# Optimization experiments

Hardware: AMD Instinct MI355X
Metric: run time of the kernel (lower is better)

## Reference

```python
import jax, jax.numpy as jnp
import numpy as np

K = 20
EPS = 1e-5


def _knn(x, k):
    # x: [B, C, N] -> indices of k nearest points, [B, N, k]
    sq = jnp.sum(x * x, axis=1)  # [B, N]
    neg_d2 = 2.0 * jnp.einsum('bcn,bcm->bnm', x, x) - sq[:, None, :] - sq[:, :, None]
    return jax.lax.top_k(neg_d2, k)[1]


def _graph_feature(x, idx):
    # x: [B, C, N], idx: [B, N, k] -> edge features [B, 2C, N, k]
    xT = x.transpose(0, 2, 1)  # [B, N, C]
    nbr = jax.vmap(lambda t, i: t[i])(xT, idx)  # [B, N, k, C]
    ctr = jnp.broadcast_to(xT[:, :, None, :], nbr.shape)
    f = jnp.concatenate([nbr - ctr, ctr], axis=-1)  # [B, N, k, 2C]
    return f.transpose(0, 3, 1, 2)


def _lrelu(x):
    return jnp.where(x > 0, x, 0.2 * x)


def _bn(x, g, b):
    # eval-mode BatchNorm with freshly-initialized running stats (mean=0, var=1)
    shp = (1, -1) + (1,) * (x.ndim - 2)
    return x * (g / jnp.sqrt(1.0 + EPS)).reshape(shp) + b.reshape(shp)


def _c2(x, w):  # 1x1 Conv2d, no bias
    return jnp.einsum('oi,bink->bonk', w, x)


def _c1(x, w):  # 1x1 Conv1d, no bias
    return jnp.einsum('oi,bin->bon', w, x)


def reference(coords, feats, w1, w2, w3, w4, w5, w6, w7, w8, w9,
              g15, b15, g6, b6, g7, b7, g8, b8):
    x0 = jnp.concatenate([coords.transpose(0, 2, 1), feats], axis=1)  # [B, 6, N]
    n = x0.shape[2]
    # EdgeConv block 1 (kNN on xyz only)
    x = _graph_feature(x0, _knn(x0[:, :3], K))  # [B, 12, N, k]
    x = _lrelu(_bn(_c2(x, w1), g15[0], b15[0]))
    x = _lrelu(_bn(_c2(x, w2), g15[1], b15[1]))
    x1 = jnp.max(x, axis=-1)  # [B, 64, N]
    # EdgeConv block 2 (dynamic kNN in feature space)
    x = _graph_feature(x1, _knn(x1, K))
    x = _lrelu(_bn(_c2(x, w3), g15[2], b15[2]))
    x = _lrelu(_bn(_c2(x, w4), g15[3], b15[3]))
    x2 = jnp.max(x, axis=-1)
    # EdgeConv block 3
    x = _graph_feature(x2, _knn(x2, K))
    x3 = jnp.max(_lrelu(_bn(_c2(x, w5), g15[4], b15[4])), axis=-1)
    # global embedding + per-point head
    xc = jnp.concatenate([x1, x2, x3], axis=1)  # [B, 192, N]
    x = _lrelu(_bn(_c1(xc, w6), g6, b6))  # [B, 1024, N]
    gmax = jnp.max(x, axis=-1, keepdims=True)
    x = jnp.concatenate([jnp.broadcast_to(gmax, (x.shape[0], x.shape[1], n)), x1, x2, x3], axis=1)  # [B,1216,N]
    x = _lrelu(_bn(_c1(x, w7), g7, b7))
    x = _lrelu(_bn(_c1(x, w8), g8, b8))
    # dropout is identity in eval mode
    x = _c1(x, w9)  # [B, 20, N]
    return x.transpose(0, 2, 1).reshape(-1, w9.shape[0])


def setup_inputs() -> dict:
    key = jax.random.key(0)
    ks = jax.random.split(key, 16)
    B, N, C = 8, 4096, 3
    s = 0.1
    return {
        'coords': jax.random.uniform(ks[0], (B, N, 3), jnp.float32),
        'feats': jax.random.normal(ks[1], (B, C, N), jnp.float32),
        'w1': s * jax.random.normal(ks[2], (64, 12), jnp.float32),
        'w2': s * jax.random.normal(ks[3], (64, 64), jnp.float32),
        'w3': s * jax.random.normal(ks[4], (64, 128), jnp.float32),
        'w4': s * jax.random.normal(ks[5], (64, 64), jnp.float32),
        'w5': s * jax.random.normal(ks[6], (64, 128), jnp.float32),
        'w6': s * jax.random.normal(ks[7], (1024, 192), jnp.float32),
        'w7': s * jax.random.normal(ks[8], (512, 1216), jnp.float32),
        'w8': s * jax.random.normal(ks[9], (256, 512), jnp.float32),
        'w9': s * jax.random.normal(ks[10], (20, 256), jnp.float32),
        'g15': jnp.ones((5, 64), jnp.float32),
        'b15': jnp.zeros((5, 64), jnp.float32),
        'g6': jnp.ones((1024,), jnp.float32),
        'b6': jnp.zeros((1024,), jnp.float32),
        'g7': jnp.ones((512,), jnp.float32),
        'b7': jnp.zeros((512,), jnp.float32),
        'g8': jnp.ones((256,), jnp.float32),
        'b8': jnp.zeros((256,), jnp.float32),
    }
```

## Files before the change

### kernel.cpp

```cpp
#include <hip/hip_runtime.h>
#include <math.h>

#define BB 8
#define NN 4096
#define KNN 20
#define EPSBN 1e-5f

__device__ __forceinline__ float lrelu(float x){ return x > 0.f ? x : 0.2f*x; }
__device__ __forceinline__ unsigned encf(float f){
  unsigned u = __float_as_uint(f);
  return (u & 0x80000000u) ? ~u : (u | 0x80000000u);
}
__device__ __forceinline__ float decf(unsigned u){
  return (u & 0x80000000u) ? __uint_as_float(u & 0x7fffffffu) : __uint_as_float(~u);
}
__device__ __forceinline__ float rdlane(float v, int l){
  return __uint_as_float(__builtin_amdgcn_readlane(__float_as_uint(v), l));
}

__global__ void prep_w(float* __restrict__ dst, const float* __restrict__ src,
                       int O, int I, int ld, int coff, const float* __restrict__ g){
  int tot = O*I;
  for(int t = blockIdx.x*blockDim.x + threadIdx.x; t < tot; t += gridDim.x*blockDim.x){
    int o = t % O, i = t / O;
    float s = g ? g[o] * (1.0f/sqrtf(1.0f+EPSBN)) : 1.0f;
    dst[(size_t)i*O + o] = src[(size_t)o*ld + coff + i] * s;
  }
}

__global__ void init_gmax(unsigned* __restrict__ g){
  int t = blockIdx.x*blockDim.x + threadIdx.x;
  if(t < BB*1024) g[t] = 0u;
}

__global__ void build_x0(const float* __restrict__ coords, const float* __restrict__ feats,
                         float* __restrict__ x0p){
  int p = blockIdx.x*blockDim.x + threadIdx.x;
  if(p >= BB*NN) return;
  int b = p / NN, n = p % NN;
  x0p[(size_t)p*6+0] = coords[(size_t)p*3+0];
  x0p[(size_t)p*6+1] = coords[(size_t)p*3+1];
  x0p[(size_t)p*6+2] = coords[(size_t)p*3+2];
  #pragma unroll
  for(int cc=0; cc<3; ++cc) x0p[(size_t)p*6+3+cc] = feats[((size_t)b*3+cc)*NN + n];
}

template<int D, int LD>
__global__ __launch_bounds__(512,4) void knn_kernel(const float* __restrict__ X, int coloff,
                                                    int* __restrict__ idxOut){
  constexpr int IG = 8;
  __shared__ float stage[2][IG][512];
  __shared__ float xi_s[IG][(D+3)&~3];
  __shared__ float sqi_s[IG];
  const int t = threadIdx.x;
  const int w = t >> 6, l = t & 63;
  const int b = blockIdx.x / (NN/IG);
  const int i0 = (blockIdx.x % (NN/IG)) * IG;
  const float* Xb = X + (size_t)b*NN*LD + coloff;

  for(int u = t; u < IG*D; u += 512) xi_s[u/D][u%D] = Xb[(size_t)(i0 + u/D)*LD + (u%D)];
  __syncthreads();
  if(t < IG){
    float s = 0.f;
    for(int d=0; d<D; ++d){ float v = xi_s[t][d]; s = fmaf(v, v, s); }
    sqi_s[t] = s;
  }
  __syncthreads();

  float v1=-INFINITY, v2=-INFINITY, v3=-INFINITY;
  int   j1=0x7fffffff, j2=0x7fffffff, j3=0x7fffffff;
  auto ins = [&](float v, int jj){
    bool b1 = v > v1, b2 = v > v2, b3 = v > v3;
    v3 = b3 ? (b2 ? v2 : v) : v3;
    j3 = b3 ? (b2 ? j2 : jj) : j3;
    v2 = b2 ? (b1 ? v1 : v) : v2;
    j2 = b2 ? (b1 ? j1 : jj) : j2;
    v1 = b1 ? v : v1;
    j1 = b1 ? jj : j1;
  };

  for(int s = 0; s < NN/512; ++s){
    const int j = s*512 + t;
    const float* row = Xb + (size_t)j*LD;
    float dot[IG];
    #pragma unroll
    for(int q=0;q<IG;++q) dot[q] = 0.f;
    float sqj = 0.f;
    if constexpr (D % 4 == 0){
      #pragma unroll
      for(int d0=0; d0<D; d0+=4){
        const float4 v = *reinterpret_cast<const float4*>(row + d0);
        sqj = fmaf(v.x,v.x,sqj); sqj = fmaf(v.y,v.y,sqj);
        sqj = fmaf(v.z,v.z,sqj); sqj = fmaf(v.w,v.w,sqj);
        #pragma unroll
        for(int q=0;q<IG;++q){
          const float4 xw = *reinterpret_cast<const float4*>(&xi_s[q][d0]);
          float a = dot[q];
          a = fmaf(v.x,xw.x,a); a = fmaf(v.y,xw.y,a);
          a = fmaf(v.z,xw.z,a); a = fmaf(v.w,xw.w,a);
          dot[q] = a;
        }
      }
    } else {
      #pragma unroll
      for(int d0=0; d0<D; ++d0){
        float v = row[d0];
        sqj = fmaf(v,v,sqj);
        #pragma unroll
        for(int q=0;q<IG;++q) dot[q] = fmaf(v, xi_s[q][d0], dot[q]);
      }
    }
    const int buf = s & 1;
    #pragma unroll
    for(int q=0;q<IG;++q)
      stage[buf][q][t] = 2.f*dot[q] - sqj - sqi_s[q];
    __syncthreads();
    {
      const float4 va = *reinterpret_cast<const float4*>(&stage[buf][w][4*l]);
      const int ja = s*512 + 4*l;
      ins(va.x, ja+0); ins(va.y, ja+1); ins(va.z, ja+2); ins(va.w, ja+3);
      const float4 vb = *reinterpret_cast<const float4*>(&stage[buf][w][256 + 4*l]);
      const int jb2 = s*512 + 256 + 4*l;
      ins(vb.x, jb2+0); ins(vb.y, jb2+1); ins(vb.z, jb2+2); ins(vb.w, jb2+3);
    }
  }

  int* outRow = idxOut + (size_t)(b*NN + i0 + w)*KNN;
  const float sqi = sqi_s[w];
  #pragma unroll 1
  for(int r=0;r<KNN;++r){
    float bv = v1; int bj = j1;
    #pragma unroll
    for(int off = 1; off < 64; off <<= 1){
      float ov = __shfl_xor(bv, off, 64);
      int oj = __shfl_xor(bj, off, 64);
      bool better = (ov > bv) || (ov == bv && oj < bj);
      bv = better ? ov : bv;
      bj = better ? oj : bj;
    }
    if(l == 0) outRow[r] = bj;
    if(((bj & 255) >> 2) == l){
      const float ve = v1; const int je = j1;
      v1=v2; j1=j2; v2=v3; j2=j3; v3=-INFINITY; j3=0x7fffffff;
      if(j1 == 0x7fffffff){
        #pragma unroll 1
        for(int s2=0; s2<NN/512; ++s2){
          #pragma unroll 1
          for(int h=0; h<2; ++h){
            #pragma unroll
            for(int e=0; e<4; ++e){
              const int jj = s2*512 + h*256 + 4*l + e;
              const float* rowp = Xb + (size_t)jj*LD;
              float dotv=0.f, sq=0.f;
              if constexpr (D % 4 == 0){
                #pragma unroll 4
                for(int d0=0; d0<D; d0+=4){
                  const float4 v = *reinterpret_cast<const float4*>(rowp + d0);
                  sq = fmaf(v.x,v.x,sq); sq = fmaf(v.y,v.y,sq);
                  sq = fmaf(v.z,v.z,sq); sq = fmaf(v.w,v.w,sq);
                  const float4 xw = *reinterpret_cast<const float4*>(&xi_s[w][d0]);
                  dotv = fmaf(v.x,xw.x,dotv); dotv = fmaf(v.y,xw.y,dotv);
                  dotv = fmaf(v.z,xw.z,dotv); dotv = fmaf(v.w,xw.w,dotv);
                }
              } else {
                #pragma unroll
                for(int d0=0; d0<D; ++d0){
                  float v = rowp[d0];
                  sq = fmaf(v,v,sq);
                  dotv = fmaf(v, xi_s[w][d0], dotv);
                }
              }
              const float dq = 2.f*dotv - sq - sqi;
              const bool ok = (dq < ve) || (dq == ve && jj > je);
              if(ok) ins(dq, jj);
            }
          }
        }
      }
    }
  }
}

template<int DIN, int NL>
__global__ __launch_bounds__(64,3) void edgeconv_k(
    const float* __restrict__ xin, int ldin, int cin_off,
    const int* __restrict__ idx,
    const float* __restrict__ WaT, const float* __restrict__ ba,
    const float* __restrict__ WbT, const float* __restrict__ bb,
    float* __restrict__ xout, int ldout, int cout_off){
  constexpr int PPB = 4;
  const int c = threadIdx.x;
  float wa[DIN];
  #pragma unroll
  for(int d=0; d<DIN; ++d) wa[d] = WaT[d*64 + c];
  float wb[(NL==2)?64:1];
  if constexpr (NL==2){
    #pragma unroll
    for(int d=0; d<64; ++d) wb[d] = WbT[d*64 + c];
  }
  const float bac = ba[c];
  const float bbc = (NL==2) ? bb[c] : 0.f;

  for(int pp=0; pp<PPB; ++pp){
    const int p = blockIdx.x*PPB + pp;
    const int b = p / NN;
    float ctr = (c < DIN) ? xin[(size_t)p*ldin + cin_off + c] : 0.f;
    float bacc[4] = {};
    #pragma unroll
    for(int d=0; d<DIN; ++d)
      bacc[d&3] += rdlane(ctr, d) * (WaT[(DIN+d)*64 + c] - wa[d]);
    const float base = bacc[0]+bacc[1]+bacc[2]+bacc[3];

    const int* irow = idx + (size_t)p*KNN;
    int myidx = (c < KNN) ? irow[c] : 0;
    float vmax = -INFINITY;
    int j0 = __builtin_amdgcn_readlane(myidx, 0);
    float nbr = (c < DIN) ? xin[(size_t)(b*NN + j0)*ldin + cin_off + c] : 0.f;
    for(int k=0; k<KNN; ++k){
      float nbrn = 0.f;
      if(k+1 < KNN){
        int jn = __builtin_amdgcn_readlane(myidx, k+1);
        nbrn = (c < DIN) ? xin[(size_t)(b*NN + jn)*ldin + cin_off + c] : 0.f;
      }
      float hacc[4] = {};
      #pragma unroll
      for(int d=0; d<DIN; ++d) hacc[d&3] += rdlane(nbr, d) * wa[d];
      float a1 = lrelu(base + hacc[0]+hacc[1]+hacc[2]+hacc[3] + bac);
      if constexpr (NL==2){
        float g[4] = {};
        #pragma unroll
        for(int d=0; d<64; ++d) g[d&3] += rdlane(a1, d) * wb[d];
        vmax = fmaxf(vmax, lrelu(g[0]+g[1]+g[2]+g[3] + bbc));
      } else {
        vmax = fmaxf(vmax, a1);
      }
      nbr = nbrn;
    }
    xout[(size_t)p*ldout + cout_off + c] = vmax;
  }
}

template<int EPI>
__global__ __launch_bounds__(256) void gemm_k(
    const float* __restrict__ A, int lda,
    const float* __restrict__ Bm, int Nw, int Ksz,
    const float* __restrict__ bias_n, const float* __restrict__ bias_bn,
    float* __restrict__ C, int ldc, unsigned* __restrict__ gmaxE){
  constexpr int ST = 68;
  __shared__ float At[32*ST];
  __shared__ float Bt[32*ST];
  const int t = threadIdx.x;
  const int m0 = blockIdx.x * 64;
  const int n0 = blockIdx.y * 64;
  const int tm = t >> 4, tn = t & 15;
  float acc[4][4] = {};
  for(int k0 = 0; k0 < Ksz; k0 += 32){
    #pragma unroll
    for(int r=0;r<2;++r){
      int lin = r*256 + t;
      int m = lin >> 3, f4 = lin & 7;
      float4 v = *reinterpret_cast<const float4*>(A + (size_t)(m0+m)*lda + k0 + f4*4);
      At[(f4*4+0)*ST + m] = v.x; At[(f4*4+1)*ST + m] = v.y;
      At[(f4*4+2)*ST + m] = v.z; At[(f4*4+3)*ST + m] = v.w;
    }
    #pragma unroll
    for(int r=0;r<2;++r){
      int lin = r*256 + t;
      int kk = lin >> 4, n4 = lin & 15;
      float4 v = *reinterpret_cast<const float4*>(Bm + (size_t)(k0+kk)*Nw + n0 + n4*4);
      *reinterpret_cast<float4*>(&Bt[kk*ST + n4*4]) = v;
    }
    __syncthreads();
    #pragma unroll
    for(int kk=0; kk<32; ++kk){
      float4 a4 = *reinterpret_cast<const float4*>(&At[kk*ST + tm*4]);
      float4 b4 = *reinterpret_cast<const float4*>(&Bt[kk*ST + tn*4]);
      float av[4] = {a4.x,a4.y,a4.z,a4.w};
      float bw[4] = {b4.x,b4.y,b4.z,b4.w};
      #pragma unroll
      for(int i2=0;i2<4;++i2)
        #pragma unroll
        for(int q=0;q<4;++q) acc[i2][q] += av[i2]*bw[q];
    }
    __syncthreads();
  }
  const int b = m0 / NN;
  if constexpr (EPI == 0){
    float* colm = At;
    #pragma unroll
    for(int q=0;q<4;++q){
      int n = n0 + tn*4 + q;
      float bn = bias_n[n];
      float mx = -INFINITY;
      #pragma unroll
      for(int r2=0;r2<4;++r2) mx = fmaxf(mx, lrelu(acc[r2][q] + bn));
      colm[tm*64 + tn*4 + q] = mx;
    }
    __syncthreads();
    if(t < 64){
      float mx = -INFINITY;
      #pragma unroll
      for(int r2=0;r2<16;++r2) mx = fmaxf(mx, colm[r2*64 + t]);
      atomicMax(gmaxE + b*1024 + n0 + t, encf(mx));
    }
  } else {
    #pragma unroll
    for(int r2=0;r2<4;++r2){
      int row = m0 + tm*4 + r2;
      float4 vo;
      float vv[4];
      #pragma unroll
      for(int q=0;q<4;++q){
        int n = n0 + tn*4 + q;
        float v = acc[r2][q];
        if constexpr (EPI == 1) v += bias_bn[b*512 + n] + bias_n[n];
        else v += bias_n[n];
        vv[q] = lrelu(v);
      }
      vo.x=vv[0]; vo.y=vv[1]; vo.z=vv[2]; vo.w=vv[3];
      *reinterpret_cast<float4*>(C + (size_t)row*ldc + n0 + tn*4) = vo;
    }
  }
}

__global__ __launch_bounds__(256) void bias7_kernel(const unsigned* __restrict__ gmaxE,
    const float* __restrict__ w7, const float* __restrict__ g7, float* __restrict__ b7p){
  __shared__ float gm[1024];
  const int t = threadIdx.x;
  const int b = blockIdx.x, half = blockIdx.y;
  for(int u=t; u<1024; u+=256) gm[u] = decf(gmaxE[b*1024+u]);
  __syncthreads();
  const int o = half*256 + t;
  const float* row = w7 + (size_t)o*1216;
  float acc = 0.f;
  for(int d0=0; d0<1024; d0+=4){
    float4 v = *reinterpret_cast<const float4*>(row + d0);
    acc += v.x*gm[d0] + v.y*gm[d0+1] + v.z*gm[d0+2] + v.w*gm[d0+3];
  }
  b7p[b*512+o] = acc * (g7[o] * (1.0f/sqrtf(1.0f+EPSBN)));
}

__global__ __launch_bounds__(64) void conv9_kernel(const float* __restrict__ y8,
    const float* __restrict__ w9, float* __restrict__ out){
  const int p = blockIdx.x*64 + threadIdx.x;
  float acc[20] = {};
  const float* row = y8 + (size_t)p*256;
  for(int d0=0; d0<256; d0+=4){
    float4 v = *reinterpret_cast<const float4*>(row + d0);
    #pragma unroll
    for(int o=0;o<20;++o){
      float4 w = *reinterpret_cast<const float4*>(w9 + o*256 + d0);
      acc[o] += v.x*w.x + v.y*w.y + v.z*w.z + v.w*w.w;
    }
  }
  #pragma unroll
  for(int o=0;o<20;++o) out[(size_t)p*20+o] = acc[o];
}

extern "C" void kernel_launch(void* const* d_in, const int* in_sizes, int n_in,
                              void* d_out, int out_size, void* d_ws, size_t ws_size,
                              hipStream_t stream){
  const float* coords = (const float*)d_in[0];
  const float* feats  = (const float*)d_in[1];
  const float* w1 = (const float*)d_in[2];
  const float* w2 = (const float*)d_in[3];
  const float* w3 = (const float*)d_in[4];
  const float* w4 = (const float*)d_in[5];
  const float* w5 = (const float*)d_in[6];
  const float* w6 = (const float*)d_in[7];
  const float* w7 = (const float*)d_in[8];
  const float* w8 = (const float*)d_in[9];
  const float* w9 = (const float*)d_in[10];
  const float* g15 = (const float*)d_in[11];
  const float* b15 = (const float*)d_in[12];
  const float* g6 = (const float*)d_in[13];
  const float* b6 = (const float*)d_in[14];
  const float* g7 = (const float*)d_in[15];
  const float* b7 = (const float*)d_in[16];
  const float* g8 = (const float*)d_in[17];
  const float* b8 = (const float*)d_in[18];
  float* out = (float*)d_out;
  float* ws = (float*)d_ws;

  size_t off = 0;
  float* xc   = ws + off; off += (size_t)BB*NN*192;
  float* x0p  = ws + off; off += (size_t)BB*NN*6;
  int*   idx  = (int*)(ws + off); off += (size_t)BB*NN*KNN;
  unsigned* gmaxE = (unsigned*)(ws + off); off += BB*1024;
  float* b7p  = ws + off; off += BB*512;
  float* w1t  = ws + off; off += 12*64;
  float* w2t  = ws + off; off += 64*64;
  float* w3t  = ws + off; off += 128*64;
  float* w4t  = ws + off; off += 64*64;
  float* w5t  = ws + off; off += 128*64;
  float* w6t  = ws + off; off += (size_t)192*1024;
  float* w7lt = ws + off; off += (size_t)192*512;
  float* w8t  = ws + off; off += (size_t)512*256;
  float* y7   = ws + off; off += (size_t)BB*NN*512;
  float* y8   = ws + off; off += (size_t)BB*NN*256;

  auto gb = [](int n){ return dim3((unsigned)((n + 255)/256)); };

  prep_w<<<gb(64*12),  256,0,stream>>>(w1t, w1, 64, 12, 12, 0, g15 + 0);
  prep_w<<<gb(64*64),  256,0,stream>>>(w2t, w2, 64, 64, 64, 0, g15 + 64);
  prep_w<<<gb(64*128), 256,0,stream>>>(w3t, w3, 64, 128, 128, 0, g15 + 128);
  prep_w<<<gb(64*64),  256,0,stream>>>(w4t, w4, 64, 64, 64, 0, g15 + 192);
  prep_w<<<gb(64*128), 256,0,stream>>>(w5t, w5, 64, 128, 128, 0, g15 + 256);
  prep_w<<<gb(1024*192),256,0,stream>>>(w6t, w6, 1024, 192, 192, 0, g6);
  prep_w<<<gb(512*192),256,0,stream>>>(w7lt, w7, 512, 192, 1216, 1024, g7);
  prep_w<<<gb(256*512),256,0,stream>>>(w8t, w8, 256, 512, 512, 0, g8);
  init_gmax<<<gb(BB*1024),256,0,stream>>>(gmaxE);
  build_x0<<<gb(BB*NN),256,0,stream>>>(coords, feats, x0p);

  knn_kernel<3,3><<<BB*(NN/8),512,0,stream>>>(coords, 0, idx);
  edgeconv_k<6,2><<<BB*NN/4,64,0,stream>>>(x0p, 6, 0, idx, w1t, b15+0, w2t, b15+64, xc, 192, 0);
  knn_kernel<64,192><<<BB*(NN/8),512,0,stream>>>(xc, 0, idx);
  edgeconv_k<64,2><<<BB*NN/4,64,0,stream>>>(xc, 192, 0, idx, w3t, b15+128, w4t, b15+192, xc, 192, 64);
  knn_kernel<64,192><<<BB*(NN/8),512,0,stream>>>(xc, 64, idx);
  edgeconv_k<64,1><<<BB*NN/4,64,0,stream>>>(xc, 192, 64, idx, w5t, b15+256, nullptr, nullptr, xc, 192, 128);

  gemm_k<0><<<dim3(BB*NN/64, 1024/64),256,0,stream>>>(xc, 192, w6t, 1024, 192, b6, nullptr, nullptr, 0, gmaxE);
  bias7_kernel<<<dim3(BB,2),256,0,stream>>>(gmaxE, w7, g7, b7p);
  gemm_k<1><<<dim3(BB*NN/64, 512/64),256,0,stream>>>(xc, 192, w7lt, 512, 192, b7, b7p, y7, 512, nullptr);
  gemm_k<2><<<dim3(BB*NN/64, 256/64),256,0,stream>>>(y7, 512, w8t, 256, 512, b8, nullptr, y8, 256, nullptr);
  conv9_kernel<<<BB*NN/64,64,0,stream>>>(y8, w9, out);
}
```

Before: 3.479 ms.

## Halve kNN block size, each thread computes two candidate rows and two queries

The kNN kernel now runs with 256 threads per block instead of 512. Each thread computes dot products for two candidate points, so the xi_s reads from shared memory are reused across two rows. Each wave then keeps top-3 lists for two query points and runs the selection and refill loop for each in turn. The aim is more arithmetic per shared-memory load and fewer block-wide syncs. The cost is higher register pressure from the doubled accumulators, and each wave must do twice as many serial selection passes.

```diff
diff --git a/kernel.cpp b/kernel.cpp
--- a/kernel.cpp
+++ b/kernel.cpp
@@ -46,7 +46,7 @@
 }
 
 template<int D, int LD>
-__global__ __launch_bounds__(512,4) void knn_kernel(const float* __restrict__ X, int coloff,
+__global__ __launch_bounds__(256,4) void knn_kernel(const float* __restrict__ X, int coloff,
                                                     int* __restrict__ idxOut){
   constexpr int IG = 8;
   __shared__ float stage[2][IG][512];
@@ -58,7 +58,7 @@
   const int i0 = (blockIdx.x % (NN/IG)) * IG;
   const float* Xb = X + (size_t)b*NN*LD + coloff;
 
-  for(int u = t; u < IG*D; u += 512) xi_s[u/D][u%D] = Xb[(size_t)(i0 + u/D)*LD + (u%D)];
+  for(int u = t; u < IG*D; u += 256) xi_s[u/D][u%D] = Xb[(size_t)(i0 + u/D)*LD + (u%D)];
   __syncthreads();
   if(t < IG){
     float s = 0.f;
@@ -67,112 +67,198 @@
   }
   __syncthreads();
 
-  float v1=-INFINITY, v2=-INFINITY, v3=-INFINITY;
-  int   j1=0x7fffffff, j2=0x7fffffff, j3=0x7fffffff;
-  auto ins = [&](float v, int jj){
-    bool b1 = v > v1, b2 = v > v2, b3 = v > v3;
-    v3 = b3 ? (b2 ? v2 : v) : v3;
-    j3 = b3 ? (b2 ? j2 : jj) : j3;
-    v2 = b2 ? (b1 ? v1 : v) : v2;
-    j2 = b2 ? (b1 ? j1 : jj) : j2;
-    v1 = b1 ? v : v1;
-    j1 = b1 ? jj : j1;
+  float vA1=-INFINITY,vA2=-INFINITY,vA3=-INFINITY;
+  int   jA1=0x7fffffff,jA2=0x7fffffff,jA3=0x7fffffff;
+  float vB1=-INFINITY,vB2=-INFINITY,vB3=-INFINITY;
+  int   jB1=0x7fffffff,jB2=0x7fffffff,jB3=0x7fffffff;
+  auto insA = [&](float v, int jj){
+    bool b1 = v > vA1, b2 = v > vA2, b3 = v > vA3;
+    vA3 = b3 ? (b2 ? vA2 : v) : vA3;  jA3 = b3 ? (b2 ? jA2 : jj) : jA3;
+    vA2 = b2 ? (b1 ? vA1 : v) : vA2;  jA2 = b2 ? (b1 ? jA1 : jj) : jA2;
+    vA1 = b1 ? v : vA1;               jA1 = b1 ? jj : jA1;
   };
+  auto insB = [&](float v, int jj){
+    bool b1 = v > vB1, b2 = v > vB2, b3 = v > vB3;
+    vB3 = b3 ? (b2 ? vB2 : v) : vB3;  jB3 = b3 ? (b2 ? jB2 : jj) : jB3;
+    vB2 = b2 ? (b1 ? vB1 : v) : vB2;  jB2 = b2 ? (b1 ? jB1 : jj) : jB2;
+    vB1 = b1 ? v : vB1;               jB1 = b1 ? jj : jB1;
+  };
+
+  const int qa = 2*w, qb = 2*w + 1;
 
   for(int s = 0; s < NN/512; ++s){
-    const int j = s*512 + t;
-    const float* row = Xb + (size_t)j*LD;
-    float dot[IG];
-    #pragma unroll
-    for(int q=0;q<IG;++q) dot[q] = 0.f;
-    float sqj = 0.f;
+    const int jA = s*512 + t;
+    const int jB = jA + 256;
+    const float* rowA = Xb + (size_t)jA*LD;
+    const float* rowB = Xb + (size_t)jB*LD;
+    float dA[IG], dB[IG];
+    #pragma unroll
+    for(int q=0;q<IG;++q){ dA[q] = 0.f; dB[q] = 0.f; }
+    float sqA = 0.f, sqB = 0.f;
     if constexpr (D % 4 == 0){
       #pragma unroll
-      for(int d0=0; d0<D; d0+=4){
-        const float4 v = *reinterpret_cast<const float4*>(row + d0);
-        sqj = fmaf(v.x,v.x,sqj); sqj = fmaf(v.y,v.y,sqj);
-        sqj = fmaf(v.z,v.z,sqj); sqj = fmaf(v.w,v.w,sqj);
+      for(int c=0; c<D/4; ++c){
+        const float4 va = *reinterpret_cast<const float4*>(rowA + c*4);
+        const float4 vb = *reinterpret_cast<const float4*>(rowB + c*4);
+        sqA = fmaf(va.x,va.x,sqA); sqA = fmaf(va.y,va.y,sqA);
+        sqA = fmaf(va.z,va.z,sqA); sqA = fmaf(va.w,va.w,sqA);
+        sqB = fmaf(vb.x,vb.x,sqB); sqB = fmaf(vb.y,vb.y,sqB);
+        sqB = fmaf(vb.z,vb.z,sqB); sqB = fmaf(vb.w,vb.w,sqB);
         #pragma unroll
         for(int q=0;q<IG;++q){
-          const float4 xw = *reinterpret_cast<const float4*>(&xi_s[q][d0]);
-          float a = dot[q];
-          a = fmaf(v.x,xw.x,a); a = fmaf(v.y,xw.y,a);
-          a = fmaf(v.z,xw.z,a); a = fmaf(v.w,xw.w,a);
-          dot[q] = a;
+          const float4 xw = *reinterpret_cast<const float4*>(&xi_s[q][c*4]);
+          float a = dA[q];
+          a = fmaf(va.x,xw.x,a); a = fmaf(va.y,xw.y,a);
+          a = fmaf(va.z,xw.z,a); a = fmaf(va.w,xw.w,a);
+          dA[q] = a;
+          float bq = dB[q];
+          bq = fmaf(vb.x,xw.x,bq); bq = fmaf(vb.y,xw.y,bq);
+          bq = fmaf(vb.z,xw.z,bq); bq = fmaf(vb.w,xw.w,bq);
+          dB[q] = bq;
         }
       }
     } else {
       #pragma unroll
       for(int d0=0; d0<D; ++d0){
-        float v = row[d0];
-        sqj = fmaf(v,v,sqj);
+        float va = rowA[d0], vb = rowB[d0];
+        sqA = fmaf(va,va,sqA);
+        sqB = fmaf(vb,vb,sqB);
         #pragma unroll
-        for(int q=0;q<IG;++q) dot[q] = fmaf(v, xi_s[q][d0], dot[q]);
+        for(int q=0;q<IG;++q){
+          float xw = xi_s[q][d0];
+          dA[q] = fmaf(va, xw, dA[q]);
+          dB[q] = fmaf(vb, xw, dB[q]);
+        }
       }
     }
     const int buf = s & 1;
     #pragma unroll
-    for(int q=0;q<IG;++q)
-      stage[buf][q][t] = 2.f*dot[q] - sqj - sqi_s[q];
+    for(int q=0;q<IG;++q){
+      stage[buf][q][t]       = 2.f*dA[q] - sqA - sqi_s[q];
+      stage[buf][q][256 + t] = 2.f*dB[q] - sqB - sqi_s[q];
+    }
     __syncthreads();
     {
-      const float4 va = *reinterpret_cast<const float4*>(&stage[buf][w][4*l]);
-      const int ja = s*512 + 4*l;
-      ins(va.x, ja+0); ins(va.y, ja+1); ins(va.z, ja+2); ins(va.w, ja+3);
-      const float4 vb = *reinterpret_cast<const float4*>(&stage[buf][w][256 + 4*l]);
-      const int jb2 = s*512 + 256 + 4*l;
-      ins(vb.x, jb2+0); ins(vb.y, jb2+1); ins(vb.z, jb2+2); ins(vb.w, jb2+3);
-    }
-  }
-
-  int* outRow = idxOut + (size_t)(b*NN + i0 + w)*KNN;
-  const float sqi = sqi_s[w];
-  #pragma unroll 1
-  for(int r=0;r<KNN;++r){
-    float bv = v1; int bj = j1;
-    #pragma unroll
-    for(int off = 1; off < 64; off <<= 1){
-      float ov = __shfl_xor(bv, off, 64);
-      int oj = __shfl_xor(bj, off, 64);
-      bool better = (ov > bv) || (ov == bv && oj < bj);
-      bv = better ? ov : bv;
-      bj = better ? oj : bj;
-    }
-    if(l == 0) outRow[r] = bj;
-    if(((bj & 255) >> 2) == l){
-      const float ve = v1; const int je = j1;
-      v1=v2; j1=j2; v2=v3; j2=j3; v3=-INFINITY; j3=0x7fffffff;
-      if(j1 == 0x7fffffff){
-        #pragma unroll 1
-        for(int s2=0; s2<NN/512; ++s2){
+      const float4 va0 = *reinterpret_cast<const float4*>(&stage[buf][qa][4*l]);
+      const int ja0 = s*512 + 4*l;
+      insA(va0.x, ja0+0); insA(va0.y, ja0+1); insA(va0.z, ja0+2); insA(va0.w, ja0+3);
+      const float4 va1 = *reinterpret_cast<const float4*>(&stage[buf][qa][256 + 4*l]);
+      const int ja1 = s*512 + 256 + 4*l;
+      insA(va1.x, ja1+0); insA(va1.y, ja1+1); insA(va1.z, ja1+2); insA(va1.w, ja1+3);
+      const float4 vb0 = *reinterpret_cast<const float4*>(&stage[buf][qb][4*l]);
+      insB(vb0.x, ja0+0); insB(vb0.y, ja0+1); insB(vb0.z, ja0+2); insB(vb0.w, ja0+3);
+      const float4 vb1 = *reinterpret_cast<const float4*>(&stage[buf][qb][256 + 4*l]);
+      insB(vb1.x, ja1+0); insB(vb1.y, ja1+1); insB(vb1.z, ja1+2); insB(vb1.w, ja1+3);
+    }
+  }
+
+  {
+    int* outRow = idxOut + (size_t)(b*NN + i0 + qa)*KNN;
+    const float sqi = sqi_s[qa];
+    #pragma unroll 1
+    for(int r=0;r<KNN;++r){
+      float bv = vA1; int bj = jA1;
+      #pragma unroll
+      for(int off = 1; off < 64; off <<= 1){
+        float ov = __shfl_xor(bv, off, 64);
+        int oj = __shfl_xor(bj, off, 64);
+        bool better = (ov > bv) || (ov == bv && oj < bj);
+        bv = better ? ov : bv;
+        bj = better ? oj : bj;
+      }
+      if(l == 0) outRow[r] = bj;
+      if(((bj & 255) >> 2) == l){
+        const float ve = vA1; const int je = jA1;
+        vA1=vA2; jA1=jA2; vA2=vA3; jA2=jA3; vA3=-INFINITY; jA3=0x7fffffff;
+        if(jA1 == 0x7fffffff){
           #pragma unroll 1
-          for(int h=0; h<2; ++h){
-            #pragma unroll
-            for(int e=0; e<4; ++e){
-              const int jj = s2*512 + h*256 + 4*l + e;
-              const float* rowp = Xb + (size_t)jj*LD;
-              float dotv=0.f, sq=0.f;
-              if constexpr (D % 4 == 0){
-                #pragma unroll 4
-                for(int d0=0; d0<D; d0+=4){
-                  const float4 v = *reinterpret_cast<const float4*>(rowp + d0);
-                  sq = fmaf(v.x,v.x,sq); sq = fmaf(v.y,v.y,sq);
-                  sq = fmaf(v.z,v.z,sq); sq = fmaf(v.w,v.w,sq);
-                  const float4 xw = *reinterpret_cast<const float4*>(&xi_s[w][d0]);
-                  dotv = fmaf(v.x,xw.x,dotv); dotv = fmaf(v.y,xw.y,dotv);
-                  dotv = fmaf(v.z,xw.z,dotv); dotv = fmaf(v.w,xw.w,dotv);
+          for(int s2=0; s2<NN/512; ++s2){
+            #pragma unroll 1
+            for(int h=0; h<2; ++h){
+              #pragma unroll
+              for(int e=0; e<4; ++e){
+                const int jj = s2*512 + h*256 + 4*l + e;
+                const float* rowp = Xb + (size_t)jj*LD;
+                float dotv=0.f, sq=0.f;
+                if constexpr (D % 4 == 0){
+                  #pragma unroll 4
+                  for(int c=0; c<D/4; ++c){
+                    const float4 v = *reinterpret_cast<const float4*>(rowp + c*4);
+                    sq = fmaf(v.x,v.x,sq); sq = fmaf(v.y,v.y,sq);
+                    sq = fmaf(v.z,v.z,sq); sq = fmaf(v.w,v.w,sq);
+                    const float4 xw = *reinterpret_cast<const float4*>(&xi_s[qa][c*4]);
+                    dotv = fmaf(v.x,xw.x,dotv); dotv = fmaf(v.y,xw.y,dotv);
+                    dotv = fmaf(v.z,xw.z,dotv); dotv = fmaf(v.w,xw.w,dotv);
+                  }
+                } else {
+                  #pragma unroll
+                  for(int d0=0; d0<D; ++d0){
+                    float v = rowp[d0];
+                    sq = fmaf(v,v,sq);
+                    dotv = fmaf(v, xi_s[qa][d0], dotv);
+                  }
                 }
-              } else {
-                #pragma unroll
-                for(int d0=0; d0<D; ++d0){
-                  float v = rowp[d0];
-                  sq = fmaf(v,v,sq);
-                  dotv = fmaf(v, xi_s[w][d0], dotv);
+                const float dq = 2.f*dotv - sq - sqi;
+                const bool ok = (dq < ve) || (dq == ve && jj > je);
+                if(ok) insA(dq, jj);
+              }
+            }
+          }
+        }
+      }
+    }
+  }
+
+  {
+    int* outRow = idxOut + (size_t)(b*NN + i0 + qb)*KNN;
+    const float sqi = sqi_s[qb];
+    #pragma unroll 1
+    for(int r=0;r<KNN;++r){
+      float bv = vB1; int bj = jB1;
+      #pragma unroll
+      for(int off = 1; off < 64; off <<= 1){
+        float ov = __shfl_xor(bv, off, 64);
+        int oj = __shfl_xor(bj, off, 64);
+        bool better = (ov > bv) || (ov == bv && oj < bj);
+        bv = better ? ov : bv;
+        bj = better ? oj : bj;
+      }
+      if(l == 0) outRow[r] = bj;
+      if(((bj & 255) >> 2) == l){
+        const float ve = vB1; const int je = jB1;
+        vB1=vB2; jB1=jB2; vB2=vB3; jB2=jB3; vB3=-INFINITY; jB3=0x7fffffff;
+        if(jB1 == 0x7fffffff){
+          #pragma unroll 1
+          for(int s2=0; s2<NN/512; ++s2){
+            #pragma unroll 1
+            for(int h=0; h<2; ++h){
+              #pragma unroll
+              for(int e=0; e<4; ++e){
+                const int jj = s2*512 + h*256 + 4*l + e;
+                const float* rowp = Xb + (size_t)jj*LD;
+                float dotv=0.f, sq=0.f;
+                if constexpr (D % 4 == 0){
+                  #pragma unroll 4
+                  for(int c=0; c<D/4; ++c){
+                    const float4 v = *reinterpret_cast<const float4*>(rowp + c*4);
+                    sq = fmaf(v.x,v.x,sq); sq = fmaf(v.y,v.y,sq);
+                    sq = fmaf(v.z,v.z,sq); sq = fmaf(v.w,v.w,sq);
+                    const float4 xw = *reinterpret_cast<const float4*>(&xi_s[qb][c*4]);
+                    dotv = fmaf(v.x,xw.x,dotv); dotv = fmaf(v.y,xw.y,dotv);
+                    dotv = fmaf(v.z,xw.z,dotv); dotv = fmaf(v.w,xw.w,dotv);
+                  }
+                } else {
+                  #pragma unroll
+                  for(int d0=0; d0<D; ++d0){
+                    float v = rowp[d0];
+                    sq = fmaf(v,v,sq);
+                    dotv = fmaf(v, xi_s[qb][d0], dotv);
+                  }
                 }
+                const float dq = 2.f*dotv - sq - sqi;
+                const bool ok = (dq < ve) || (dq == ve && jj > je);
+                if(ok) insB(dq, jj);
               }
-              const float dq = 2.f*dotv - sq - sqi;
-              const bool ok = (dq < ve) || (dq == ve && jj > je);
-              if(ok) ins(dq, jj);
             }
           }
         }
@@ -412,11 +498,11 @@
   init_gmax<<<gb(BB*1024),256,0,stream>>>(gmaxE);
   build_x0<<<gb(BB*NN),256,0,stream>>>(coords, feats, x0p);
 
-  knn_kernel<3,3><<<BB*(NN/8),512,0,stream>>>(coords, 0, idx);
+  knn_kernel<3,3><<<BB*(NN/8),256,0,stream>>>(coords, 0, idx);
   edgeconv_k<6,2><<<BB*NN/4,64,0,stream>>>(x0p, 6, 0, idx, w1t, b15+0, w2t, b15+64, xc, 192, 0);
-  knn_kernel<64,192><<<BB*(NN/8),512,0,stream>>>(xc, 0, idx);
+  knn_kernel<64,192><<<BB*(NN/8),256,0,stream>>>(xc, 0, idx);
   edgeconv_k<64,2><<<BB*NN/4,64,0,stream>>>(xc, 192, 0, idx, w3t, b15+128, w4t, b15+192, xc, 192, 64);
-  knn_kernel<64,192><<<BB*(NN/8),512,0,stream>>>(xc, 64, idx);
+  knn_kernel<64,192><<<BB*(NN/8),256,0,stream>>>(xc, 64, idx);
   edgeconv_k<64,1><<<BB*NN/4,64,0,stream>>>(xc, 192, 64, idx, w5t, b15+256, nullptr, nullptr, xc, 192, 128);
 
   gemm_k<0><<<dim3(BB*NN/64, 1024/64),256,0,stream>>>(xc, 192, w6t, 1024, 192, b6, nullptr, nullptr, 0, gmaxE);
```

After: 3.778 ms. 1.09x slower.
